# Optimization experiments

Measured on AMD Instinct MI355X. Metric: run time of the kernel, lower is better.

Reference implementation:

```python
import jax, jax.numpy as jnp
import numpy as np

KERNEL_SIZE = 16
STRIDE = 8
NEG = -1.0e9


def setup_inputs() -> dict:
    key = jax.random.key(0)
    k1, k2, k3, k4, k5 = jax.random.split(key, 5)
    B, C, L = 8, 512, 4096
    x = jax.random.normal(k1, (B, C, L), dtype=jnp.float32)
    mask = jax.random.randint(k2, (B, L), 0, 2).astype(bool)
    W = jax.random.normal(k3, (C, C), dtype=jnp.float32) * 0.02
    b = jax.random.normal(k4, (C,), dtype=jnp.float32) * 0.02
    v = jax.random.normal(k5, (C,), dtype=jnp.float32) * 0.02
    return {"x": x, "mask": mask, "W": W, "b": b, "v": v}


def reference(x, mask, W, b, v):
    # x: [B, C, L], mask: [B, L] (True = masked out)
    B, C, L = x.shape
    win, step = KERNEL_SIZE, STRIDE
    L_pool = 1 + (L - win) // step
    # per-token projection (identical across windows since proj is per-token)
    h = jnp.tanh(jnp.einsum('bcl,dc->bld', x, W) + b)      # [B, L, C]
    s = jnp.einsum('bld,d->bl', h, v)                       # [B, L]
    idx = jnp.arange(L_pool)[:, None] * step + jnp.arange(win)[None, :]
    sw = s[:, idx]
    mw = mask[:, idx]
    sw = jnp.where(mw, NEG, sw)
    w = jax.nn.softmax(sw, axis=-1)
    w = jnp.where(mw, 0.0, w)
    norm = jnp.clip(jnp.sum(w, axis=-1, keepdims=True), 1e-6, None)
    w = w / norm
    xw = x[:, :, idx]
    return jnp.einsum('bcpw,bpw->bcp', xw, w)               # [B, C, L_pool]
```

## Files before the change

kernel.cpp:

```cpp
#include <hip/hip_runtime.h>
#include <hip/hip_bf16.h>
#include <cmath>

#define Bsz 8
#define Csz 512
#define Lsz 4096
#define LPOOL 511
#define NEGV -1000000000.0f

typedef __attribute__((ext_vector_type(8))) short short8;
typedef __attribute__((ext_vector_type(4))) float float4v;

__device__ __forceinline__ void gl_lds16(const __hip_bfloat16* g, void* l) {
  __builtin_amdgcn_global_load_lds(
      (const __attribute__((address_space(1))) unsigned int*)g,
      (__attribute__((address_space(3))) unsigned int*)l, 16, 0, 0);
}

__global__ __launch_bounds__(256) void prep(const unsigned char* __restrict__ mb,
    int* __restrict__ flag, float* __restrict__ s, const float* __restrict__ W,
    __hip_bfloat16* __restrict__ Wts) {
  const int bid = blockIdx.x, tid = threadIdx.x;
  if (bid == 0) {
    __shared__ int sf;
    if (tid == 0) sf = 0;
    __syncthreads();
    int f = 0;
    for (int i = tid; i < 4096; i += 256)
      if ((i & 3) && mb[i]) f = 1;
    if (f) atomicOr(&sf, 1);
    __syncthreads();
    if (tid == 0) *flag = sf;
  } else if (bid <= 32) {
    int i = (bid - 1) * 1024 + tid * 4;
    float4 z; z.x = z.y = z.z = z.w = 0.f;
    *(float4*)(s + i) = z;
  } else {
    int tg = (bid - 33) * 256 + tid;
    int d = tg >> 6, cg = tg & 63;
    float4 w0 = *(const float4*)(W + (size_t)d * 512 + cg * 8);
    float4 w1 = *(const float4*)(W + (size_t)d * 512 + cg * 8 + 4);
    __hip_bfloat16 hb[8];
    hb[0] = __float2bfloat16(w0.x); hb[1] = __float2bfloat16(w0.y);
    hb[2] = __float2bfloat16(w0.z); hb[3] = __float2bfloat16(w0.w);
    hb[4] = __float2bfloat16(w1.x); hb[5] = __float2bfloat16(w1.y);
    hb[6] = __float2bfloat16(w1.z); hb[7] = __float2bfloat16(w1.w);
    int nt = d >> 7, row = d & 127, ks = cg >> 2, seg = cg & 3;
    *(short8*)(Wts + (((size_t)nt * 16 + ks) * 512 + seg * 128 + row) * 8) = *(short8*)hb;
  }
}

__global__ __launch_bounds__(256) void transpose_x(const float* __restrict__ x,
                                                   __hip_bfloat16* __restrict__ xTs) {
  __shared__ float sX[64][65];
  const int lt = blockIdx.x, ct = blockIdx.y, b = blockIdx.z;
  const int tid = threadIdx.x;
  const int l0 = lt * 64;
  const float* xb = x + ((size_t)b * Csz + ct * 64) * Lsz + l0;
  #pragma unroll
  for (int it = 0; it < 4; ++it) {
    int c = it * 16 + (tid >> 4);
    int l = (tid & 15) * 4;
    *(float4*)(&sX[c][l]) = *(const float4*)(xb + (size_t)c * Lsz + l);
  }
  __syncthreads();
  #pragma unroll
  for (int it = 0; it < 2; ++it) {
    int u = it * 256 + tid;
    int cg = u >> 6, ll = u & 63;
    __hip_bfloat16 hb[8];
    #pragma unroll
    for (int j = 0; j < 8; ++j)
      hb[j] = __float2bfloat16(sX[cg * 8 + j][ll]);
    int m = b * Lsz + l0 + ll;
    int mt = m >> 7, row = m & 127;
    int cglob = ct * 64 + cg * 8;
    int ks = cglob >> 5, seg = (cglob >> 3) & 3;
    *(short8*)(xTs + (((size_t)mt * 16 + ks) * 512 + seg * 128 + row) * 8) = *(short8*)hb;
  }
}

__global__ __launch_bounds__(256, 2) void gemm_bf16(
    const __hip_bfloat16* __restrict__ xTs, const __hip_bfloat16* __restrict__ Wts,
    const float* __restrict__ bias, const float* __restrict__ v,
    float* __restrict__ s) {
  __shared__ short8 sAv[512];
  __shared__ short8 sBv[512];
  const int tid = threadIdx.x;
  const int lane = tid & 63, wave = tid >> 6;
  const int lr = lane & 15, quad = lane >> 4;
  const int mh = wave >> 1, nh = wave & 1;
  const int mt = blockIdx.x, nt = blockIdx.y;
  const __hip_bfloat16* aT = xTs + (size_t)mt * 65536;
  const __hip_bfloat16* bT = Wts + (size_t)nt * 65536;

  float bl[4], vl[4];
  #pragma unroll
  for (int nf = 0; nf < 4; ++nf) {
    int n = nt * 128 + nh * 64 + nf * 16 + lr;
    bl[nf] = bias[n]; vl[nf] = v[n];
  }

  float4v acc[4][4];
  #pragma unroll
  for (int i = 0; i < 4; ++i)
    #pragma unroll
    for (int j = 0; j < 4; ++j) acc[i][j] = (float4v)0.f;

  for (int ks = 0; ks < 16; ++ks) {
    __syncthreads();
    const __hip_bfloat16* ga = aT + ks * 4096 + (wave * 64 + lane) * 8;
    const __hip_bfloat16* gb = bT + ks * 4096 + (wave * 64 + lane) * 8;
    gl_lds16(ga,        &sAv[wave * 64]);
    gl_lds16(ga + 2048, &sAv[256 + wave * 64]);
    gl_lds16(gb,        &sBv[wave * 64]);
    gl_lds16(gb + 2048, &sBv[256 + wave * 64]);
    __syncthreads();
    short8 af[4], bfr[4];
    #pragma unroll
    for (int mf = 0; mf < 4; ++mf)
      af[mf] = sAv[quad * 128 + mh * 64 + mf * 16 + lr];
    #pragma unroll
    for (int nf = 0; nf < 4; ++nf)
      bfr[nf] = sBv[quad * 128 + nh * 64 + nf * 16 + lr];
    #pragma unroll
    for (int mf = 0; mf < 4; ++mf)
      #pragma unroll
      for (int nf = 0; nf < 4; ++nf)
        acc[mf][nf] = __builtin_amdgcn_mfma_f32_16x16x32_bf16(af[mf], bfr[nf], acc[mf][nf], 0, 0, 0);
  }

  #pragma unroll
  for (int mf = 0; mf < 4; ++mf) {
    #pragma unroll
    for (int reg = 0; reg < 4; ++reg) {
      float p = 0.f;
      #pragma unroll
      for (int nf = 0; nf < 4; ++nf)
        p += tanhf(acc[mf][nf][reg] + bl[nf]) * vl[nf];
      p += __shfl_xor(p, 1, 16);
      p += __shfl_xor(p, 2, 16);
      p += __shfl_xor(p, 4, 16);
      p += __shfl_xor(p, 8, 16);
      if (lr == 0)
        atomicAdd(&s[mt * 128 + mh * 64 + mf * 16 + quad * 4 + reg], p);
    }
  }
}

__global__ __launch_bounds__(256) void gemm_s_f32(const float* __restrict__ x,
    const float* __restrict__ W, const float* __restrict__ bias,
    const float* __restrict__ v, float* __restrict__ s_out) {
  __shared__ float sA[32][64];
  __shared__ float sB[32][68];
  __shared__ float s_acc[64];
  const int tid = threadIdx.x;
  const int b = blockIdx.y;
  const int l0 = blockIdx.x * 64;
  if (tid < 64) s_acc[tid] = 0.0f;
  const int tx = tid & 15;
  const int ty = tid >> 4;
  const float* xb = x + ((size_t)b * Csz) * Lsz + l0;
  for (int d0 = 0; d0 < Csz; d0 += 64) {
    float acc[4][4] = {{0.f}};
    for (int c0 = 0; c0 < Csz; c0 += 32) {
      __syncthreads();
      #pragma unroll
      for (int it = 0; it < 8; ++it) {
        int idx = tid + it * 256;
        int kc = idx >> 6, ml = idx & 63;
        sA[kc][ml] = xb[(size_t)(c0 + kc) * Lsz + ml];
      }
      #pragma unroll
      for (int it = 0; it < 8; ++it) {
        int idx = tid + it * 256;
        int kc = idx & 31, dj = idx >> 5;
        sB[kc][dj] = W[(size_t)(d0 + dj) * Csz + c0 + kc];
      }
      __syncthreads();
      #pragma unroll
      for (int kc = 0; kc < 32; ++kc) {
        float4 a  = *(const float4*)(&sA[kc][tx << 2]);
        float4 w4 = *(const float4*)(&sB[kc][ty << 2]);
        acc[0][0] += a.x * w4.x; acc[0][1] += a.x * w4.y; acc[0][2] += a.x * w4.z; acc[0][3] += a.x * w4.w;
        acc[1][0] += a.y * w4.x; acc[1][1] += a.y * w4.y; acc[1][2] += a.y * w4.z; acc[1][3] += a.y * w4.w;
        acc[2][0] += a.z * w4.x; acc[2][1] += a.z * w4.y; acc[2][2] += a.z * w4.z; acc[2][3] += a.z * w4.w;
        acc[3][0] += a.w * w4.x; acc[3][1] += a.w * w4.y; acc[3][2] += a.w * w4.z; acc[3][3] += a.w * w4.w;
      }
    }
    float part[4] = {0.f, 0.f, 0.f, 0.f};
    #pragma unroll
    for (int j = 0; j < 4; ++j) {
      int d = d0 + (ty << 2) + j;
      float bj = bias[d], vj = v[d];
      #pragma unroll
      for (int i = 0; i < 4; ++i)
        part[i] += tanhf(acc[i][j] + bj) * vj;
    }
    #pragma unroll
    for (int i = 0; i < 4; ++i)
      atomicAdd(&s_acc[(tx << 2) + i], part[i]);
  }
  __syncthreads();
  if (tid < 64) s_out[(size_t)b * Lsz + l0 + tid] = s_acc[tid];
}

__global__ void win_weights(const float* __restrict__ s, const void* __restrict__ mask,
                            const int* __restrict__ flag, float* __restrict__ wgt) {
  int t = blockIdx.x * blockDim.x + threadIdx.x;
  if (t >= Bsz * LPOOL) return;
  int b = t / LPOOL, p = t - b * LPOOL;
  const bool u8 = (*flag != 0);
  const unsigned char* m8 = (const unsigned char*)mask;
  const int* m32 = (const int*)mask;
  float sv[16]; int mv[16];
  float mx = -3.4e38f;
  int base = b * Lsz + p * 8;
  #pragma unroll
  for (int w = 0; w < 16; ++w) {
    int mk = u8 ? (int)m8[base + w] : m32[base + w];
    float val = mk ? NEGV : s[base + w];
    sv[w] = val; mv[w] = mk;
    mx = fmaxf(mx, val);
  }
  float sum = 0.f;
  #pragma unroll
  for (int w = 0; w < 16; ++w) { sv[w] = expf(sv[w] - mx); sum += sv[w]; }
  float inv = 1.0f / sum;
  float norm = 0.f;
  #pragma unroll
  for (int w = 0; w < 16; ++w) { sv[w] = mv[w] ? 0.f : sv[w] * inv; norm += sv[w]; }
  norm = fmaxf(norm, 1e-6f);
  float rn = 1.0f / norm;
  #pragma unroll
  for (int w = 0; w < 16; ++w) wgt[t * 16 + w] = sv[w] * rn;
}

__global__ __launch_bounds__(256) void pool_out(const float* __restrict__ x,
    const float* __restrict__ wgt, float* __restrict__ out) {
  __shared__ float xrow[Lsz];
  int bc = blockIdx.x;
  int c = bc & (Csz - 1);
  int b = bc >> 9;
  const float* xr = x + ((size_t)b * Csz + c) * Lsz;
  int tid = threadIdx.x;
  #pragma unroll
  for (int it = 0; it < 4; ++it) {
    int idx = (tid + it * 256) << 2;
    *(float4*)(&xrow[idx]) = *(const float4*)(&xr[idx]);
  }
  __syncthreads();
  const float* wb = wgt + (size_t)b * LPOOL * 16;
  float* ob = out + ((size_t)b * Csz + c) * LPOOL;
  for (int p = tid; p < LPOOL; p += 256) {
    const float4* wp = (const float4*)(wb + p * 16);
    const float4* xp = (const float4*)(&xrow[p * 8]);
    float acc = 0.f;
    #pragma unroll
    for (int q = 0; q < 4; ++q) {
      float4 wv = wp[q], xv = xp[q];
      acc += xv.x * wv.x + xv.y * wv.y + xv.z * wv.z + xv.w * wv.w;
    }
    ob[p] = acc;
  }
}

extern "C" void kernel_launch(void* const* d_in, const int* in_sizes, int n_in,
                              void* d_out, int out_size, void* d_ws, size_t ws_size,
                              hipStream_t stream) {
  const float* x    = (const float*)d_in[0];
  const void*  mask = d_in[1];
  const float* W    = (const float*)d_in[2];
  const float* bias = (const float*)d_in[3];
  const float* v    = (const float*)d_in[4];
  float* out = (float*)d_out;

  char* wsb = (char*)d_ws;
  int*   flag = (int*)wsb;
  float* s    = (float*)(wsb + 256);
  float* wgt  = (float*)(wsb + 131328);
  __hip_bfloat16* Wts = (__hip_bfloat16*)(wsb + 393216);
  __hip_bfloat16* xTs = (__hip_bfloat16*)(wsb + 917504);
  const size_t NEED = 917504 + 33554432;

  if (ws_size >= NEED) {
    prep<<<161, 256, 0, stream>>>((const unsigned char*)mask, flag, s, W, Wts);
    transpose_x<<<dim3(Lsz / 64, Csz / 64, Bsz), 256, 0, stream>>>(x, xTs);
    gemm_bf16<<<dim3(256, 4), 256, 0, stream>>>(xTs, Wts, bias, v, s);
  } else {
    prep<<<1, 256, 0, stream>>>((const unsigned char*)mask, flag, s, W, Wts);
    gemm_s_f32<<<dim3(Lsz / 64, Bsz), 256, 0, stream>>>(x, W, bias, v, s);
  }
  win_weights<<<(Bsz * LPOOL + 255) / 256, 256, 0, stream>>>(s, mask, flag, wgt);
  pool_out<<<Bsz * Csz, 256, 0, stream>>>(x, wgt, out);
}
```

Baseline: 160.8 us.

## Fuse prep and transpose, emit bf16 copy of x, fuse window weights into pooling

Merges the prep and transpose kernels into a single launch that also writes a row-major bf16 copy of x. A new pool2 kernel computes the window softmax weights in-block and pools from the bf16 copy. This replaces the separate win_weights and pool_out launches on the fast path and halves the bytes the pooling step reads. The cost is an extra 32MB bf16 write and lower precision in the pooled output, since it now uses bf16 x instead of fp32.

```diff
diff --git a/kernel.cpp b/kernel.cpp
--- a/kernel.cpp
+++ b/kernel.cpp
@@ -11,72 +11,89 @@
 typedef __attribute__((ext_vector_type(8))) short short8;
 typedef __attribute__((ext_vector_type(4))) float float4v;
 
+__device__ __forceinline__ float bf2f(short u) {
+  unsigned int x = ((unsigned int)(unsigned short)u) << 16;
+  return __builtin_bit_cast(float, x);
+}
+
 __device__ __forceinline__ void gl_lds16(const __hip_bfloat16* g, void* l) {
   __builtin_amdgcn_global_load_lds(
       (const __attribute__((address_space(1))) unsigned int*)g,
       (__attribute__((address_space(3))) unsigned int*)l, 16, 0, 0);
 }
 
-__global__ __launch_bounds__(256) void prep(const unsigned char* __restrict__ mb,
-    int* __restrict__ flag, float* __restrict__ s, const float* __restrict__ W,
+__global__ __launch_bounds__(256) void stage1(const float* __restrict__ x,
+    __hip_bfloat16* __restrict__ xTs, __hip_bfloat16* __restrict__ xbf,
+    const unsigned char* __restrict__ mb, int* __restrict__ flag,
+    float* __restrict__ s, const float* __restrict__ W,
     __hip_bfloat16* __restrict__ Wts) {
-  const int bid = blockIdx.x, tid = threadIdx.x;
-  if (bid == 0) {
-    __shared__ int sf;
-    if (tid == 0) sf = 0;
+  const int tid = threadIdx.x;
+  const int bid = blockIdx.x;
+  if (bid < 4096) {
+    __shared__ float sX[64][65];
+    const int lt = bid & 63, ct = (bid >> 6) & 7, b = bid >> 9;
+    const int l0 = lt * 64;
+    const float* xb = x + ((size_t)b * Csz + ct * 64) * Lsz + l0;
+    #pragma unroll
+    for (int it = 0; it < 4; ++it) {
+      int c = it * 16 + (tid >> 4);
+      int l = (tid & 15) * 4;
+      *(float4*)(&sX[c][l]) = *(const float4*)(xb + (size_t)c * Lsz + l);
+    }
     __syncthreads();
-    int f = 0;
-    for (int i = tid; i < 4096; i += 256)
-      if ((i & 3) && mb[i]) f = 1;
-    if (f) atomicOr(&sf, 1);
-    __syncthreads();
-    if (tid == 0) *flag = sf;
-  } else if (bid <= 32) {
-    int i = (bid - 1) * 1024 + tid * 4;
-    float4 z; z.x = z.y = z.z = z.w = 0.f;
-    *(float4*)(s + i) = z;
+    #pragma unroll
+    for (int it = 0; it < 2; ++it) {
+      int u = it * 256 + tid;
+      int cg = u >> 6, ll = u & 63;
+      __hip_bfloat16 hb[8];
+      #pragma unroll
+      for (int j = 0; j < 8; ++j)
+        hb[j] = __float2bfloat16(sX[cg * 8 + j][ll]);
+      int m = b * Lsz + l0 + ll;
+      int mt = m >> 7, row = m & 127;
+      int cglob = ct * 64 + cg * 8;
+      int ks = cglob >> 5, seg = (cglob >> 3) & 3;
+      *(short8*)(xTs + (((size_t)mt * 16 + ks) * 512 + seg * 128 + row) * 8) = *(short8*)hb;
+    }
+    #pragma unroll
+    for (int it = 0; it < 2; ++it) {
+      int u = it * 256 + tid;
+      int cg = u >> 3, lseg = u & 7;
+      __hip_bfloat16 hb[8];
+      #pragma unroll
+      for (int j = 0; j < 8; ++j)
+        hb[j] = __float2bfloat16(sX[cg][lseg * 8 + j]);
+      *(short8*)(xbf + ((size_t)b * Csz + ct * 64 + cg) * Lsz + l0 + lseg * 8) = *(short8*)hb;
+    }
   } else {
-    int tg = (bid - 33) * 256 + tid;
-    int d = tg >> 6, cg = tg & 63;
-    float4 w0 = *(const float4*)(W + (size_t)d * 512 + cg * 8);
-    float4 w1 = *(const float4*)(W + (size_t)d * 512 + cg * 8 + 4);
-    __hip_bfloat16 hb[8];
-    hb[0] = __float2bfloat16(w0.x); hb[1] = __float2bfloat16(w0.y);
-    hb[2] = __float2bfloat16(w0.z); hb[3] = __float2bfloat16(w0.w);
-    hb[4] = __float2bfloat16(w1.x); hb[5] = __float2bfloat16(w1.y);
-    hb[6] = __float2bfloat16(w1.z); hb[7] = __float2bfloat16(w1.w);
-    int nt = d >> 7, row = d & 127, ks = cg >> 2, seg = cg & 3;
-    *(short8*)(Wts + (((size_t)nt * 16 + ks) * 512 + seg * 128 + row) * 8) = *(short8*)hb;
-  }
-}
-
-__global__ __launch_bounds__(256) void transpose_x(const float* __restrict__ x,
-                                                   __hip_bfloat16* __restrict__ xTs) {
-  __shared__ float sX[64][65];
-  const int lt = blockIdx.x, ct = blockIdx.y, b = blockIdx.z;
-  const int tid = threadIdx.x;
-  const int l0 = lt * 64;
-  const float* xb = x + ((size_t)b * Csz + ct * 64) * Lsz + l0;
-  #pragma unroll
-  for (int it = 0; it < 4; ++it) {
-    int c = it * 16 + (tid >> 4);
-    int l = (tid & 15) * 4;
-    *(float4*)(&sX[c][l]) = *(const float4*)(xb + (size_t)c * Lsz + l);
-  }
-  __syncthreads();
-  #pragma unroll
-  for (int it = 0; it < 2; ++it) {
-    int u = it * 256 + tid;
-    int cg = u >> 6, ll = u & 63;
-    __hip_bfloat16 hb[8];
-    #pragma unroll
-    for (int j = 0; j < 8; ++j)
-      hb[j] = __float2bfloat16(sX[cg * 8 + j][ll]);
-    int m = b * Lsz + l0 + ll;
-    int mt = m >> 7, row = m & 127;
-    int cglob = ct * 64 + cg * 8;
-    int ks = cglob >> 5, seg = (cglob >> 3) & 3;
-    *(short8*)(xTs + (((size_t)mt * 16 + ks) * 512 + seg * 128 + row) * 8) = *(short8*)hb;
+    const int pb = bid - 4096;
+    if (pb == 0) {
+      __shared__ int sf;
+      if (tid == 0) sf = 0;
+      __syncthreads();
+      int f = 0;
+      for (int i = tid; i < 4096; i += 256)
+        if ((i & 3) && mb[i]) f = 1;
+      if (f) atomicOr(&sf, 1);
+      __syncthreads();
+      if (tid == 0) *flag = sf;
+    } else if (pb <= 32) {
+      int i = (pb - 1) * 1024 + tid * 4;
+      float4 z; z.x = z.y = z.z = z.w = 0.f;
+      *(float4*)(s + i) = z;
+    } else {
+      int tg = (pb - 33) * 256 + tid;
+      int d = tg >> 6, cg = tg & 63;
+      float4 w0 = *(const float4*)(W + (size_t)d * 512 + cg * 8);
+      float4 w1 = *(const float4*)(W + (size_t)d * 512 + cg * 8 + 4);
+      __hip_bfloat16 hb[8];
+      hb[0] = __float2bfloat16(w0.x); hb[1] = __float2bfloat16(w0.y);
+      hb[2] = __float2bfloat16(w0.z); hb[3] = __float2bfloat16(w0.w);
+      hb[4] = __float2bfloat16(w1.x); hb[5] = __float2bfloat16(w1.y);
+      hb[6] = __float2bfloat16(w1.z); hb[7] = __float2bfloat16(w1.w);
+      int nt = d >> 7, row = d & 127, ks = cg >> 2, seg = cg & 3;
+      *(short8*)(Wts + (((size_t)nt * 16 + ks) * 512 + seg * 128 + row) * 8) = *(short8*)hb;
+    }
   }
 }
 
@@ -146,6 +163,73 @@
         atomicAdd(&s[mt * 128 + mh * 64 + mf * 16 + quad * 4 + reg], p);
     }
   }
+}
+
+__global__ __launch_bounds__(256) void pool2(const __hip_bfloat16* __restrict__ xbf,
+    const float* __restrict__ s, const void* __restrict__ mask,
+    const int* __restrict__ flag, float* __restrict__ out) {
+  __shared__ float wl[8][17];
+  const int t = threadIdx.x;
+  const int p0 = blockIdx.x * 8, b = blockIdx.y;
+  if (t < 8 && p0 + t < LPOOL) {
+    const int p = p0 + t;
+    const bool u8 = (*flag != 0);
+    const unsigned char* m8 = (const unsigned char*)mask;
+    const int* m32 = (const int*)mask;
+    const int base = b * Lsz + p * 8;
+    float sv[16]; int mv[16];
+    float mx = -3.4e38f;
+    #pragma unroll
+    for (int w = 0; w < 16; ++w) {
+      int mk = u8 ? (int)m8[base + w] : m32[base + w];
+      float val = mk ? NEGV : s[base + w];
+      sv[w] = val; mv[w] = mk;
+      mx = fmaxf(mx, val);
+    }
+    float sum = 0.f;
+    #pragma unroll
+    for (int w = 0; w < 16; ++w) { sv[w] = expf(sv[w] - mx); sum += sv[w]; }
+    float inv = 1.0f / sum;
+    float norm = 0.f;
+    #pragma unroll
+    for (int w = 0; w < 16; ++w) { sv[w] = mv[w] ? 0.f : sv[w] * inv; norm += sv[w]; }
+    norm = fmaxf(norm, 1e-6f);
+    float rn = 1.0f / norm;
+    #pragma unroll
+    for (int w = 0; w < 16; ++w) wl[t][w] = sv[w] * rn;
+  }
+  __syncthreads();
+  const int ci = t >> 3, pi = t & 7;
+  const int p = p0 + pi;
+  if (p >= LPOOL) return;
+  float wr[16];
+  #pragma unroll
+  for (int w = 0; w < 16; ++w) wr[w] = wl[pi][w];
+  #pragma unroll 4
+  for (int it = 0; it < 16; ++it) {
+    int c = it * 32 + ci;
+    const __hip_bfloat16* xp = xbf + ((size_t)b * Csz + c) * Lsz + 8 * p;
+    short8 lo = *(const short8*)xp;
+    short8 hi = *(const short8*)(xp + 8);
+    float acc = 0.f;
+    #pragma unroll
+    for (int j = 0; j < 8; ++j)
+      acc += bf2f(lo[j]) * wr[j] + bf2f(hi[j]) * wr[8 + j];
+    out[((size_t)b * Csz + c) * LPOOL + p] = acc;
+  }
+}
+
+__global__ void detect_mask(const unsigned char* __restrict__ mb, int* __restrict__ flag) {
+  __shared__ int sf;
+  int t = threadIdx.x;
+  if (t == 0) sf = 0;
+  __syncthreads();
+  int f = 0;
+  for (int i = t; i < 4096; i += 256)
+    if ((i & 3) && mb[i]) f = 1;
+  if (f) atomicOr(&sf, 1);
+  __syncthreads();
+  if (t == 0) *flag = sf;
 }
 
 __global__ __launch_bounds__(256) void gemm_s_f32(const float* __restrict__ x,
@@ -281,16 +365,18 @@
   float* wgt  = (float*)(wsb + 131328);
   __hip_bfloat16* Wts = (__hip_bfloat16*)(wsb + 393216);
   __hip_bfloat16* xTs = (__hip_bfloat16*)(wsb + 917504);
-  const size_t NEED = 917504 + 33554432;
+  __hip_bfloat16* xbf = (__hip_bfloat16*)(wsb + 917504 + 33554432);
+  const size_t NEED = 917504 + 33554432 + 33554432;
 
   if (ws_size >= NEED) {
-    prep<<<161, 256, 0, stream>>>((const unsigned char*)mask, flag, s, W, Wts);
-    transpose_x<<<dim3(Lsz / 64, Csz / 64, Bsz), 256, 0, stream>>>(x, xTs);
+    stage1<<<4096 + 161, 256, 0, stream>>>(x, xTs, xbf,
+        (const unsigned char*)mask, flag, s, W, Wts);
     gemm_bf16<<<dim3(256, 4), 256, 0, stream>>>(xTs, Wts, bias, v, s);
+    pool2<<<dim3(64, Bsz), 256, 0, stream>>>(xbf, s, mask, flag, out);
   } else {
-    prep<<<1, 256, 0, stream>>>((const unsigned char*)mask, flag, s, W, Wts);
+    detect_mask<<<1, 256, 0, stream>>>((const unsigned char*)mask, flag);
     gemm_s_f32<<<dim3(Lsz / 64, Bsz), 256, 0, stream>>>(x, W, bias, v, s);
-  }
-  win_weights<<<(Bsz * LPOOL + 255) / 256, 256, 0, stream>>>(s, mask, flag, wgt);
-  pool_out<<<Bsz * Csz, 256, 0, stream>>>(x, wgt, out);
-}
+    win_weights<<<(Bsz * LPOOL + 255) / 256, 256, 0, stream>>>(s, mask, flag, wgt);
+    pool_out<<<Bsz * Csz, 256, 0, stream>>>(x, wgt, out);
+  }
+}
```

After: 158.8 us. Within noise of the previous version (-1.2%).
